# Kernel optimization log

Hardware: AMD Instinct MI355X
Metric: run time of the kernel (lower is better)

## Reference

```python
import jax, jax.numpy as jnp
import numpy as np

GROUPS = 32
EPS = 1e-5

def group_norm(x, w, b):
    # x: [B, C, T]
    B, C, T = x.shape
    g = x.reshape(B, GROUPS, C // GROUPS, T)
    mu = g.mean(axis=(2, 3), keepdims=True)
    var = g.var(axis=(2, 3), keepdims=True)
    g = (g - mu) * jax.lax.rsqrt(var + EPS)
    return g.reshape(B, C, T) * w[None, :, None] + b[None, :, None]

def conv1x1(x, w, b):
    # x: [B, C, T], w: [O, C], b: [O]
    return jnp.einsum('oc,bct->bot', w, x) + b[None, :, None]

def setup_inputs() -> dict:
    key = jax.random.key(0)
    ks = jax.random.split(key, 10)
    B, C, H, W = 128, 512, 16, 16
    d = {}
    d['criminal_cond'] = jax.random.normal(ks[0], (B, C, H, W), jnp.float32)
    d['morph_cond'] = jax.random.normal(ks[1], (B, C, H, W), jnp.float32)
    d['norm_w'] = jax.random.uniform(ks[2], (C,), jnp.float32, 0.5, 1.5)
    d['norm_b'] = 0.02 * jax.random.normal(ks[3], (C,), jnp.float32)
    d['qkv_w'] = jax.random.normal(ks[4], (3 * C, C), jnp.float32) / np.sqrt(C)
    d['qkv_b'] = 0.02 * jax.random.normal(ks[5], (3 * C,), jnp.float32)
    d['ekv_w'] = jax.random.normal(ks[6], (2 * C, C), jnp.float32) / np.sqrt(C)
    d['ekv_b'] = 0.02 * jax.random.normal(ks[7], (2 * C,), jnp.float32)
    d['proj_w'] = jax.random.normal(ks[8], (C, C), jnp.float32) / np.sqrt(C)
    d['proj_b'] = 0.02 * jax.random.normal(ks[9], (C,), jnp.float32)
    return d

def reference(criminal_cond, morph_cond, norm_w, norm_b, qkv_w, qkv_b, ekv_w, ekv_b, proj_w, proj_b):
    B, C, H, W = criminal_cond.shape
    x = criminal_cond.reshape(B, C, H * W)          # [B, C, T]
    cond = morph_cond.reshape(B, C, H * W)          # [B, C, S], S == T here
    h = group_norm(x, norm_w, norm_b)
    qkv = conv1x1(h, qkv_w, qkv_b)                  # [B, 3C, T]
    q, k, v = jnp.split(qkv, 3, axis=1)
    ekv = conv1x1(cond, ekv_w, ekv_b)               # [B, 2C, S]
    ek, ev = jnp.split(ekv, 2, axis=1)
    k = jnp.concatenate([ek, k], axis=-1)           # [B, C, S+T]
    v = jnp.concatenate([ev, v], axis=-1)
    scale = 1.0 / np.sqrt(np.sqrt(C))               # single head, head_dim = C
    logits = jnp.einsum('bct,bcs->bts', q * scale, k * scale)
    w = jax.nn.softmax(logits, axis=-1)             # [B, T, S+T]
    a = jnp.einsum('bts,bcs->bct', w, v)            # [B, C, T]
    hout = conv1x1(a, proj_w, proj_b)
    attn_out = (x + hout).reshape(B, C, H, W)
    return 2.0 * morph_cond - attn_out
```

## Files before the change

### kernel.cpp

```cpp
#include <hip/hip_runtime.h>
#include <hip/hip_bf16.h>
#include <math.h>

#define NB 128
#define NC 512
#define NT 256
#define NL 512
#define NG 32
#define SCALE2 0.04419417382415922f

typedef __attribute__((ext_vector_type(8))) short bf16x8;
typedef __attribute__((ext_vector_type(4))) float f32x4;
typedef __attribute__((ext_vector_type(4))) unsigned short u16x4;
typedef __attribute__((ext_vector_type(8))) unsigned short u16x8;
typedef __hip_bfloat16 bf16;

struct Params {
  const float *x, *morph, *qkvb, *ekvb, *projb;
  const bf16 *wq, *we, *wp;
  bf16 *hT, *mT, *qT, *kfT, *vf;
  float *out;
  int b0;
};

__device__ inline unsigned short f2bf_bits(float f) {
  bf16 h = __float2bfloat16(f);
  return *reinterpret_cast<unsigned short*>(&h);
}

__device__ inline void gld16(const void* g, void* lds) {
  __builtin_amdgcn_global_load_lds(
      (const __attribute__((address_space(1))) unsigned int*)g,
      (__attribute__((address_space(3))) unsigned int*)lds, 16, 0, 0);
}

__global__ __launch_bounds__(256) void gn_stats_k(const float* __restrict__ x,
                                                  float* __restrict__ stats) {
  const int bg = blockIdx.x;
  const float4* p4 = (const float4*)(x + (size_t)bg * 4096);
  float s = 0.f, s2 = 0.f;
  #pragma unroll
  for (int i = 0; i < 4; ++i) {
    float4 v = p4[threadIdx.x + i * 256];
    s  += v.x + v.y + v.z + v.w;
    s2 += v.x * v.x + v.y * v.y + v.z * v.z + v.w * v.w;
  }
  #pragma unroll
  for (int off = 32; off; off >>= 1) {
    s  += __shfl_down(s, off);
    s2 += __shfl_down(s2, off);
  }
  __shared__ float red[8];
  const int wave = threadIdx.x >> 6, lane = threadIdx.x & 63;
  if (lane == 0) { red[wave * 2] = s; red[wave * 2 + 1] = s2; }
  __syncthreads();
  if (threadIdx.x == 0) {
    float S = 0.f, S2 = 0.f;
    for (int w = 0; w < 4; ++w) { S += red[w * 2]; S2 += red[w * 2 + 1]; }
    float mu = S * (1.0f / 4096.0f);
    float var = S2 * (1.0f / 4096.0f) - mu * mu;
    stats[bg * 2]     = mu;
    stats[bg * 2 + 1] = rsqrtf(var + 1e-5f);
  }
}

__global__ __launch_bounds__(256) void cvt_k(const float* __restrict__ s,
                                             bf16* __restrict__ d, int n) {
  int i = blockIdx.x * 256 + threadIdx.x;
  if (i < n) d[i] = __float2bfloat16(s[i]);
}

__global__ __launch_bounds__(256) void transpose2_k(const float* __restrict__ x,
                                                    const float* __restrict__ morph,
                                                    bf16* __restrict__ hT,
                                                    bf16* __restrict__ mT,
                                                    const float* __restrict__ stats,
                                                    const float* __restrict__ gnw,
                                                    const float* __restrict__ gnb,
                                                    int b0, int nbc) {
  __shared__ float sm[64][65];
  const int z = blockIdx.z;
  const int norm = (z < nbc) ? 1 : 0;
  const int lb = norm ? z : z - nbc;
  const int gb = b0 + lb;
  const float* src = norm ? x : morph;
  bf16* dst = norm ? hT : mT;
  const int t0 = blockIdx.x * 64, c0 = blockIdx.y * 64;
  const int tx = threadIdx.x & 15, ty = threadIdx.x >> 4;
  #pragma unroll
  for (int ci = 0; ci < 4; ++ci) {
    const int c = ty + ci * 16;
    const int cg = c0 + c;
    float4 v = *(const float4*)&src[((size_t)gb * NC + cg) * NT + t0 + tx * 4];
    if (norm) {
      float mu = stats[(gb * NG + (cg >> 4)) * 2];
      float rs = stats[(gb * NG + (cg >> 4)) * 2 + 1];
      float wv = gnw[cg], bv = gnb[cg];
      v.x = (v.x - mu) * rs * wv + bv;
      v.y = (v.y - mu) * rs * wv + bv;
      v.z = (v.z - mu) * rs * wv + bv;
      v.w = (v.w - mu) * rs * wv + bv;
    }
    sm[c][tx * 4 + 0] = v.x; sm[c][tx * 4 + 1] = v.y;
    sm[c][tx * 4 + 2] = v.z; sm[c][tx * 4 + 3] = v.w;
  }
  __syncthreads();
  const int t = threadIdx.x >> 2, cq = threadIdx.x & 3;
  u16x8 pk0, pk1;
  #pragma unroll
  for (int k = 0; k < 8; ++k) pk0[k] = f2bf_bits(sm[cq * 16 + k][t]);
  #pragma unroll
  for (int k = 0; k < 8; ++k) pk1[k] = f2bf_bits(sm[cq * 16 + 8 + k][t]);
  bf16* d = dst + ((size_t)lb * NT + t0 + t) * NC + c0 + cq * 16;
  *(u16x8*)d = pk0;
  *(u16x8*)(d + 8) = pk1;
}

__global__ __launch_bounds__(256) void gemm_in_k(Params P) {
  __shared__ unsigned short As[128][32];
  __shared__ unsigned short Bs[128][32];
  const int lb = blockIdx.x;
  const int m0 = blockIdx.y * 128;
  const int z = blockIdx.z;
  const bool qkv = (z < 12);
  const int n0 = (qkv ? z : z - 12) * 128;
  const int tid = threadIdx.x;
  const int lane = tid & 63, w = tid >> 6;
  const int wr = w >> 1, wc = w & 1;
  const int ln = lane & 15, kq = lane >> 4;

  const bf16* Ab = (qkv ? P.hT : P.mT) + (size_t)lb * NT * NC;
  const bf16* Bb = qkv ? P.wq : P.we;

  const char* Abase = (const char*)(Ab + (size_t)m0 * 512);
  const char* Bbase = (const char*)(Bb + (size_t)n0 * 512);

  const int r_lo = w * 32 + (lane >> 2);
  const int cid16 = (lane & 3) * 16;

  f32x4 acc[4][4] = {};

  for (int k0 = 0; k0 < 512; k0 += 32) {
    const size_t kb = (size_t)k0 * 2 + cid16;
    #pragma unroll
    for (int h = 0; h < 2; ++h) {
      const int rw = r_lo + h * 16;
      gld16(Abase + (size_t)rw * 1024 + kb, (char*)As + w * 2048 + h * 1024);
      gld16(Bbase + (size_t)rw * 1024 + kb, (char*)Bs + w * 2048 + h * 1024);
    }
    __syncthreads();
    bf16x8 af[4], bfr[4];
    #pragma unroll
    for (int i = 0; i < 4; ++i)
      af[i] = *(const bf16x8*)&As[wr * 64 + i * 16 + ln][kq * 8];
    #pragma unroll
    for (int j = 0; j < 4; ++j)
      bfr[j] = *(const bf16x8*)&Bs[wc * 64 + j * 16 + ln][kq * 8];
    #pragma unroll
    for (int i = 0; i < 4; ++i)
      #pragma unroll
      for (int j = 0; j < 4; ++j)
        acc[i][j] = __builtin_amdgcn_mfma_f32_16x16x32_bf16(af[i], bfr[j], acc[i][j], 0, 0, 0);
    __syncthreads();
  }

  #pragma unroll
  for (int i = 0; i < 4; ++i) {
    const int ig = m0 + wr * 64 + i * 16 + kq * 4;
    #pragma unroll
    for (int j = 0; j < 4; ++j) {
      const int jg = n0 + wc * 64 + j * 16 + ln;
      f32x4 a = acc[i][j];
      if (qkv) {
        float bias = P.qkvb[jg];
        if (jg < 512) {
          bf16* d = P.qT + ((size_t)lb * NT + ig) * NC + jg;
          #pragma unroll
          for (int r = 0; r < 4; ++r) d[(size_t)r * NC] = __float2bfloat16(a[r] + bias);
        } else if (jg < 1024) {
          bf16* d = P.kfT + ((size_t)lb * NL + 256 + ig) * NC + (jg - 512);
          #pragma unroll
          for (int r = 0; r < 4; ++r) d[(size_t)r * NC] = __float2bfloat16(a[r] + bias);
        } else {
          u16x4 pk;
          #pragma unroll
          for (int r = 0; r < 4; ++r) pk[r] = f2bf_bits(a[r] + bias);
          *(u16x4*)(P.vf + ((size_t)lb * NC + (jg - 1024)) * NL + 256 + ig) = pk;
        }
      } else {
        float bias = P.ekvb[jg];
        if (jg < 512) {
          bf16* d = P.kfT + ((size_t)lb * NL + ig) * NC + jg;
          #pragma unroll
          for (int r = 0; r < 4; ++r) d[(size_t)r * NC] = __float2bfloat16(a[r] + bias);
        } else {
          u16x4 pk;
          #pragma unroll
          for (int r = 0; r < 4; ++r) pk[r] = f2bf_bits(a[r] + bias);
          *(u16x4*)(P.vf + ((size_t)lb * NC + (jg - 512)) * NL + ig) = pk;
        }
      }
    }
  }
}

__global__ __launch_bounds__(256) void att_sm_k(Params P) {
  __shared__ unsigned short Abuf[32][32];
  __shared__ unsigned short Bbuf[512][32];
  __shared__ float redm[4][32];
  __shared__ float reds[4][32];

  const int lb = blockIdx.x;
  const int t0 = blockIdx.y * 32;
  const int tid = threadIdx.x;
  const int lane = tid & 63, w = tid >> 6;
  const int ln = lane & 15, kq = lane >> 4;
  const int srow = lane >> 2;
  const int scol = (lane & 3) * 16;

  const char* qg = (const char*)(P.qT  + ((size_t)lb * NT + t0) * NC);
  const char* kg = (const char*)(P.kfT + (size_t)lb * NL * NC);

  f32x4 sa[2][8] = {};
  bf16x8 af[2], bfr[8];

  for (int k0 = 0; k0 < 512; k0 += 32) {
    const size_t koff = (size_t)k0 * 2 + scol;
    if (w < 2)
      gld16(qg + (size_t)(w * 16 + srow) * 1024 + koff, (char*)Abuf + w * 1024);
    #pragma unroll
    for (int h = 0; h < 8; ++h)
      gld16(kg + (size_t)(w * 128 + h * 16 + srow) * 1024 + koff,
            (char*)Bbuf + w * 8192 + h * 1024);
    __syncthreads();
    af[0] = *(const bf16x8*)&Abuf[ln][kq * 8];
    af[1] = *(const bf16x8*)&Abuf[16 + ln][kq * 8];
    #pragma unroll
    for (int j = 0; j < 8; ++j)
      bfr[j] = *(const bf16x8*)&Bbuf[w * 128 + j * 16 + ln][kq * 8];
    #pragma unroll
    for (int i = 0; i < 2; ++i)
      #pragma unroll
      for (int j = 0; j < 8; ++j)
        sa[i][j] = __builtin_amdgcn_mfma_f32_16x16x32_bf16(af[i], bfr[j], sa[i][j], 0, 0, 0);
    __syncthreads();
  }

  float mx[2][4], sum[2][4], inv[2][4];
  #pragma unroll
  for (int i = 0; i < 2; ++i)
    #pragma unroll
    for (int r = 0; r < 4; ++r) {
      float m = -1e30f;
      #pragma unroll
      for (int j = 0; j < 8; ++j) m = fmaxf(m, sa[i][j][r]);
      mx[i][r] = m;
    }
  #pragma unroll
  for (int off = 1; off < 16; off <<= 1)
    #pragma unroll
    for (int i = 0; i < 2; ++i)
      #pragma unroll
      for (int r = 0; r < 4; ++r) mx[i][r] = fmaxf(mx[i][r], __shfl_xor(mx[i][r], off));
  if (ln == 0)
    #pragma unroll
    for (int i = 0; i < 2; ++i)
      #pragma unroll
      for (int r = 0; r < 4; ++r) redm[w][i * 16 + kq * 4 + r] = mx[i][r];
  __syncthreads();
  #pragma unroll
  for (int i = 0; i < 2; ++i)
    #pragma unroll
    for (int r = 0; r < 4; ++r) {
      const int row = i * 16 + kq * 4 + r;
      mx[i][r] = fmaxf(fmaxf(redm[0][row], redm[1][row]),
                       fmaxf(redm[2][row], redm[3][row]));
      sum[i][r] = 0.f;
    }
  #pragma unroll
  for (int i = 0; i < 2; ++i)
    #pragma unroll
    for (int j = 0; j < 8; ++j)
      #pragma unroll
      for (int r = 0; r < 4; ++r) {
        float e = __expf(SCALE2 * (sa[i][j][r] - mx[i][r]));
        sa[i][j][r] = e;
        sum[i][r] += e;
      }
  #pragma unroll
  for (int off = 1; off < 16; off <<= 1)
    #pragma unroll
    for (int i = 0; i < 2; ++i)
      #pragma unroll
      for (int r = 0; r < 4; ++r) sum[i][r] += __shfl_xor(sum[i][r], off);
  if (ln == 0)
    #pragma unroll
    for (int i = 0; i < 2; ++i)
      #pragma unroll
      for (int r = 0; r < 4; ++r) reds[w][i * 16 + kq * 4 + r] = sum[i][r];
  __syncthreads();
  #pragma unroll
  for (int i = 0; i < 2; ++i)
    #pragma unroll
    for (int r = 0; r < 4; ++r) {
      const int row = i * 16 + kq * 4 + r;
      inv[i][r] = 1.0f / (reds[0][row] + reds[1][row] + reds[2][row] + reds[3][row]);
    }

  bf16* pdst = P.qT + ((size_t)lb * NT + t0) * NL;
  #pragma unroll
  for (int i = 0; i < 2; ++i)
    #pragma unroll
    for (int j = 0; j < 8; ++j)
      #pragma unroll
      for (int r = 0; r < 4; ++r)
        pdst[(size_t)(i * 16 + kq * 4 + r) * NL + w * 128 + j * 16 + ln] =
            __float2bfloat16(sa[i][j][r] * inv[i][r]);
}

template <int MODE>
__global__ __launch_bounds__(256) void gemm_att(Params P) {
  __shared__ unsigned short As[128][32];
  __shared__ unsigned short Bs[128][32];
  const int lb = blockIdx.x;
  const int m0 = blockIdx.y * 128;
  const int n0 = blockIdx.z * 128;
  const int tid = threadIdx.x;
  const int lane = tid & 63, w = tid >> 6;
  const int wr = w >> 1, wc = w & 1;
  const int ln = lane & 15, kq = lane >> 4;

  const bf16 *Ab, *Bb;
  if (MODE == 1) { Ab = P.qT  + (size_t)lb * 131072; Bb = P.vf + (size_t)lb * NC * NL; }
  else           { Ab = P.kfT + (size_t)lb * 262144; Bb = P.wp; }

  const char* Abase = (const char*)(Ab + (size_t)m0 * 512);
  const char* Bbase = (const char*)(Bb + (size_t)n0 * 512);

  const int r_lo = w * 32 + (lane >> 2);
  const int cid16 = (lane & 3) * 16;

  f32x4 acc[4][4] = {};

  for (int k0 = 0; k0 < 512; k0 += 32) {
    const size_t kb = (size_t)k0 * 2 + cid16;
    #pragma unroll
    for (int h = 0; h < 2; ++h) {
      const int rw = r_lo + h * 16;
      gld16(Abase + (size_t)rw * 1024 + kb, (char*)As + w * 2048 + h * 1024);
      gld16(Bbase + (size_t)rw * 1024 + kb, (char*)Bs + w * 2048 + h * 1024);
    }
    __syncthreads();
    bf16x8 af[4], bfr[4];
    #pragma unroll
    for (int i = 0; i < 4; ++i)
      af[i] = *(const bf16x8*)&As[wr * 64 + i * 16 + ln][kq * 8];
    #pragma unroll
    for (int j = 0; j < 4; ++j)
      bfr[j] = *(const bf16x8*)&Bs[wc * 64 + j * 16 + ln][kq * 8];
    #pragma unroll
    for (int i = 0; i < 4; ++i)
      #pragma unroll
      for (int j = 0; j < 4; ++j)
        acc[i][j] = __builtin_amdgcn_mfma_f32_16x16x32_bf16(af[i], bfr[j], acc[i][j], 0, 0, 0);
    __syncthreads();
  }

  bf16* Og = P.kfT + (size_t)lb * 262144;
  const int gb = P.b0 + lb;

  #pragma unroll
  for (int i = 0; i < 4; ++i) {
    const int ig = m0 + wr * 64 + i * 16 + kq * 4;
    #pragma unroll
    for (int j = 0; j < 4; ++j) {
      const int jg = n0 + wc * 64 + j * 16 + ln;
      f32x4 a = acc[i][j];
      if (MODE == 1) {
        bf16* d = Og + (size_t)ig * NC + jg;
        #pragma unroll
        for (int r = 0; r < 4; ++r) d[(size_t)r * NC] = __float2bfloat16(a[r]);
      } else {
        const float bias = P.projb[jg];
        const size_t idx = ((size_t)gb * NC + jg) * NT + ig;
        float4 mo = *(const float4*)&P.morph[idx];
        float4 xx = *(const float4*)&P.x[idx];
        f32x4 o;
        o[0] = 2.0f * mo.x - xx.x - (a[0] + bias);
        o[1] = 2.0f * mo.y - xx.y - (a[1] + bias);
        o[2] = 2.0f * mo.z - xx.z - (a[2] + bias);
        o[3] = 2.0f * mo.w - xx.w - (a[3] + bias);
        *(f32x4*)&P.out[idx] = o;
      }
    }
  }
}

extern "C" void kernel_launch(void* const* d_in, const int* in_sizes, int n_in,
                              void* d_out, int out_size, void* d_ws, size_t ws_size,
                              hipStream_t stream) {
  const float* x     = (const float*)d_in[0];
  const float* morph = (const float*)d_in[1];
  const float* gnw   = (const float*)d_in[2];
  const float* gnb   = (const float*)d_in[3];
  const float* qkvw  = (const float*)d_in[4];
  const float* qkvb  = (const float*)d_in[5];
  const float* ekvw  = (const float*)d_in[6];
  const float* ekvb  = (const float*)d_in[7];
  const float* projw = (const float*)d_in[8];
  const float* projb = (const float*)d_in[9];

  bf16* wq = (bf16*)d_ws;
  bf16* we = wq + 786432;
  bf16* wp = we + 524288;
  float* stats = (float*)(wp + 262144);
  bf16* pb = (bf16*)(stats + 8192);

  const size_t per_b = 917504;
  const size_t fixed = (size_t)(786432 + 524288 + 262144) * 2 + 8192 * 4;
  int nbc = NB;
  while (nbc > 1 && fixed + (size_t)nbc * per_b * 2 > ws_size) nbc >>= 1;

  Params P;
  P.x = x; P.morph = morph; P.qkvb = qkvb; P.ekvb = ekvb; P.projb = projb;
  P.wq = wq; P.we = we; P.wp = wp;
  P.hT  = pb;  pb += (size_t)nbc * 131072;
  P.mT  = pb;  pb += (size_t)nbc * 131072;
  P.qT  = pb;  pb += (size_t)nbc * 131072;
  P.kfT = pb;  pb += (size_t)nbc * 262144;
  P.vf  = pb;
  P.out = (float*)d_out;

  gn_stats_k<<<dim3(NB * NG), dim3(256), 0, stream>>>(x, stats);
  cvt_k<<<dim3(3072), dim3(256), 0, stream>>>(qkvw, wq, 786432);
  cvt_k<<<dim3(2048), dim3(256), 0, stream>>>(ekvw, we, 524288);
  cvt_k<<<dim3(1024), dim3(256), 0, stream>>>(projw, wp, 262144);

  for (int b0 = 0; b0 < NB; b0 += nbc) {
    P.b0 = b0;
    transpose2_k<<<dim3(4, 8, 2 * nbc), dim3(256), 0, stream>>>(
        x, morph, P.hT, P.mT, stats, gnw, gnb, b0, nbc);
    gemm_in_k  <<<dim3(nbc, 2, 20), dim3(256), 0, stream>>>(P);
    att_sm_k   <<<dim3(nbc, 8),     dim3(256), 0, stream>>>(P);
    gemm_att<1><<<dim3(nbc, 2, 4),  dim3(256), 0, stream>>>(P);
    gemm_att<2><<<dim3(nbc, 2, 4),  dim3(256), 0, stream>>>(P);
  }
}
```

Measured before the change: 537.0 us.

## Double-buffer LDS tiles in GEMM kernels to overlap global loads with MFMA

Result: slower. 565.7 us (+5.3%).

```diff
diff --git a/kernel.cpp b/kernel.cpp
--- a/kernel.cpp
+++ b/kernel.cpp
@@ -117,8 +117,8 @@
 }
 
 __global__ __launch_bounds__(256) void gemm_in_k(Params P) {
-  __shared__ unsigned short As[128][32];
-  __shared__ unsigned short Bs[128][32];
+  __shared__ unsigned short As[2][128][32];
+  __shared__ unsigned short Bs[2][128][32];
   const int lb = blockIdx.x;
   const int m0 = blockIdx.y * 128;
   const int z = blockIdx.z;
@@ -140,22 +140,33 @@
 
   f32x4 acc[4][4] = {};
 
-  for (int k0 = 0; k0 < 512; k0 += 32) {
-    const size_t kb = (size_t)k0 * 2 + cid16;
-    #pragma unroll
-    for (int h = 0; h < 2; ++h) {
-      const int rw = r_lo + h * 16;
-      gld16(Abase + (size_t)rw * 1024 + kb, (char*)As + w * 2048 + h * 1024);
-      gld16(Bbase + (size_t)rw * 1024 + kb, (char*)Bs + w * 2048 + h * 1024);
-    }
-    __syncthreads();
+  #pragma unroll
+  for (int h = 0; h < 2; ++h) {
+    const int rw = r_lo + h * 16;
+    gld16(Abase + (size_t)rw * 1024 + cid16, (char*)As[0] + w * 2048 + h * 1024);
+    gld16(Bbase + (size_t)rw * 1024 + cid16, (char*)Bs[0] + w * 2048 + h * 1024);
+  }
+  __syncthreads();
+
+  #pragma unroll
+  for (int t = 0; t < 16; ++t) {
+    const int cur = t & 1, nxt = cur ^ 1;
+    if (t < 15) {
+      const size_t kb = (size_t)(t + 1) * 64 + cid16;
+      #pragma unroll
+      for (int h = 0; h < 2; ++h) {
+        const int rw = r_lo + h * 16;
+        gld16(Abase + (size_t)rw * 1024 + kb, (char*)As[nxt] + w * 2048 + h * 1024);
+        gld16(Bbase + (size_t)rw * 1024 + kb, (char*)Bs[nxt] + w * 2048 + h * 1024);
+      }
+    }
     bf16x8 af[4], bfr[4];
     #pragma unroll
     for (int i = 0; i < 4; ++i)
-      af[i] = *(const bf16x8*)&As[wr * 64 + i * 16 + ln][kq * 8];
+      af[i] = *(const bf16x8*)&As[cur][wr * 64 + i * 16 + ln][kq * 8];
     #pragma unroll
     for (int j = 0; j < 4; ++j)
-      bfr[j] = *(const bf16x8*)&Bs[wc * 64 + j * 16 + ln][kq * 8];
+      bfr[j] = *(const bf16x8*)&Bs[cur][wc * 64 + j * 16 + ln][kq * 8];
     #pragma unroll
     for (int i = 0; i < 4; ++i)
       #pragma unroll
@@ -320,8 +331,8 @@
 
 template <int MODE>
 __global__ __launch_bounds__(256) void gemm_att(Params P) {
-  __shared__ unsigned short As[128][32];
-  __shared__ unsigned short Bs[128][32];
+  __shared__ unsigned short As[2][128][32];
+  __shared__ unsigned short Bs[2][128][32];
   const int lb = blockIdx.x;
   const int m0 = blockIdx.y * 128;
   const int n0 = blockIdx.z * 128;
@@ -342,22 +353,33 @@
 
   f32x4 acc[4][4] = {};
 
-  for (int k0 = 0; k0 < 512; k0 += 32) {
-    const size_t kb = (size_t)k0 * 2 + cid16;
-    #pragma unroll
-    for (int h = 0; h < 2; ++h) {
-      const int rw = r_lo + h * 16;
-      gld16(Abase + (size_t)rw * 1024 + kb, (char*)As + w * 2048 + h * 1024);
-      gld16(Bbase + (size_t)rw * 1024 + kb, (char*)Bs + w * 2048 + h * 1024);
-    }
-    __syncthreads();
+  #pragma unroll
+  for (int h = 0; h < 2; ++h) {
+    const int rw = r_lo + h * 16;
+    gld16(Abase + (size_t)rw * 1024 + cid16, (char*)As[0] + w * 2048 + h * 1024);
+    gld16(Bbase + (size_t)rw * 1024 + cid16, (char*)Bs[0] + w * 2048 + h * 1024);
+  }
+  __syncthreads();
+
+  #pragma unroll
+  for (int t = 0; t < 16; ++t) {
+    const int cur = t & 1, nxt = cur ^ 1;
+    if (t < 15) {
+      const size_t kb = (size_t)(t + 1) * 64 + cid16;
+      #pragma unroll
+      for (int h = 0; h < 2; ++h) {
+        const int rw = r_lo + h * 16;
+        gld16(Abase + (size_t)rw * 1024 + kb, (char*)As[nxt] + w * 2048 + h * 1024);
+        gld16(Bbase + (size_t)rw * 1024 + kb, (char*)Bs[nxt] + w * 2048 + h * 1024);
+      }
+    }
     bf16x8 af[4], bfr[4];
     #pragma unroll
     for (int i = 0; i < 4; ++i)
-      af[i] = *(const bf16x8*)&As[wr * 64 + i * 16 + ln][kq * 8];
+      af[i] = *(const bf16x8*)&As[cur][wr * 64 + i * 16 + ln][kq * 8];
     #pragma unroll
     for (int j = 0; j < 4; ++j)
-      bfr[j] = *(const bf16x8*)&Bs[wc * 64 + j * 16 + ln][kq * 8];
+      bfr[j] = *(const bf16x8*)&Bs[cur][wc * 64 + j * 16 + ln][kq * 8];
     #pragma unroll
     for (int i = 0; i < 4; ++i)
       #pragma unroll
```

## Double GEMM K-tile to 64 with XOR-swizzled LDS and fuse weight casts

Applied to the files above, without the earlier changes.

Result: slower. 553.5 us (+3.1%).

```diff
diff --git a/kernel.cpp b/kernel.cpp
--- a/kernel.cpp
+++ b/kernel.cpp
@@ -64,10 +64,18 @@
   }
 }
 
-__global__ __launch_bounds__(256) void cvt_k(const float* __restrict__ s,
-                                             bf16* __restrict__ d, int n) {
-  int i = blockIdx.x * 256 + threadIdx.x;
-  if (i < n) d[i] = __float2bfloat16(s[i]);
+__global__ __launch_bounds__(256) void cvt3_k(const float* __restrict__ a,
+                                              const float* __restrict__ b,
+                                              const float* __restrict__ c,
+                                              bf16* __restrict__ da,
+                                              bf16* __restrict__ db,
+                                              bf16* __restrict__ dc) {
+  const int i = blockIdx.x * 256 + threadIdx.x;
+  if (i < 786432) { da[i] = __float2bfloat16(a[i]); return; }
+  const int j = i - 786432;
+  if (j < 524288) { db[j] = __float2bfloat16(b[j]); return; }
+  const int k = j - 524288;
+  if (k < 262144) dc[k] = __float2bfloat16(c[k]);
 }
 
 __global__ __launch_bounds__(256) void transpose2_k(const float* __restrict__ x,
@@ -117,8 +125,8 @@
 }
 
 __global__ __launch_bounds__(256) void gemm_in_k(Params P) {
-  __shared__ unsigned short As[128][32];
-  __shared__ unsigned short Bs[128][32];
+  __shared__ unsigned short As[128][64];
+  __shared__ unsigned short Bs[128][64];
   const int lb = blockIdx.x;
   const int m0 = blockIdx.y * 128;
   const int z = blockIdx.z;
@@ -131,36 +139,40 @@
 
   const bf16* Ab = (qkv ? P.hT : P.mT) + (size_t)lb * NT * NC;
   const bf16* Bb = qkv ? P.wq : P.we;
-
   const char* Abase = (const char*)(Ab + (size_t)m0 * 512);
   const char* Bbase = (const char*)(Bb + (size_t)n0 * 512);
 
-  const int r_lo = w * 32 + (lane >> 2);
-  const int cid16 = (lane & 3) * 16;
+  const int r8 = lane >> 3;
+  const int ssl = (lane & 7) ^ r8;
+  const int xr = ln & 7;
 
   f32x4 acc[4][4] = {};
 
-  for (int k0 = 0; k0 < 512; k0 += 32) {
-    const size_t kb = (size_t)k0 * 2 + cid16;
-    #pragma unroll
-    for (int h = 0; h < 2; ++h) {
-      const int rw = r_lo + h * 16;
-      gld16(Abase + (size_t)rw * 1024 + kb, (char*)As + w * 2048 + h * 1024);
-      gld16(Bbase + (size_t)rw * 1024 + kb, (char*)Bs + w * 2048 + h * 1024);
-    }
-    __syncthreads();
-    bf16x8 af[4], bfr[4];
-    #pragma unroll
-    for (int i = 0; i < 4; ++i)
-      af[i] = *(const bf16x8*)&As[wr * 64 + i * 16 + ln][kq * 8];
-    #pragma unroll
-    for (int j = 0; j < 4; ++j)
-      bfr[j] = *(const bf16x8*)&Bs[wc * 64 + j * 16 + ln][kq * 8];
-    #pragma unroll
-    for (int i = 0; i < 4; ++i)
+  for (int k0 = 0; k0 < 512; k0 += 64) {
+    #pragma unroll
+    for (int h = 0; h < 4; ++h) {
+      const int rw = w * 32 + h * 8 + r8;
+      const size_t goff = (size_t)rw * 1024 + (size_t)k0 * 2 + ssl * 16;
+      gld16(Abase + goff, (char*)As + (w * 32 + h * 8) * 128);
+      gld16(Bbase + goff, (char*)Bs + (w * 32 + h * 8) * 128);
+    }
+    __syncthreads();
+    #pragma unroll
+    for (int hf = 0; hf < 2; ++hf) {
+      const int sl = ((hf * 4 + kq) ^ xr) * 8;
+      bf16x8 af[4], bfr[4];
+      #pragma unroll
+      for (int i = 0; i < 4; ++i)
+        af[i] = *(const bf16x8*)&As[wr * 64 + i * 16 + ln][sl];
       #pragma unroll
       for (int j = 0; j < 4; ++j)
-        acc[i][j] = __builtin_amdgcn_mfma_f32_16x16x32_bf16(af[i], bfr[j], acc[i][j], 0, 0, 0);
+        bfr[j] = *(const bf16x8*)&Bs[wc * 64 + j * 16 + ln][sl];
+      #pragma unroll
+      for (int i = 0; i < 4; ++i)
+        #pragma unroll
+        for (int j = 0; j < 4; ++j)
+          acc[i][j] = __builtin_amdgcn_mfma_f32_16x16x32_bf16(af[i], bfr[j], acc[i][j], 0, 0, 0);
+    }
     __syncthreads();
   }
 
@@ -320,8 +332,8 @@
 
 template <int MODE>
 __global__ __launch_bounds__(256) void gemm_att(Params P) {
-  __shared__ unsigned short As[128][32];
-  __shared__ unsigned short Bs[128][32];
+  __shared__ unsigned short As[128][64];
+  __shared__ unsigned short Bs[128][64];
   const int lb = blockIdx.x;
   const int m0 = blockIdx.y * 128;
   const int n0 = blockIdx.z * 128;
@@ -337,32 +349,37 @@
   const char* Abase = (const char*)(Ab + (size_t)m0 * 512);
   const char* Bbase = (const char*)(Bb + (size_t)n0 * 512);
 
-  const int r_lo = w * 32 + (lane >> 2);
-  const int cid16 = (lane & 3) * 16;
+  const int r8 = lane >> 3;
+  const int ssl = (lane & 7) ^ r8;
+  const int xr = ln & 7;
 
   f32x4 acc[4][4] = {};
 
-  for (int k0 = 0; k0 < 512; k0 += 32) {
-    const size_t kb = (size_t)k0 * 2 + cid16;
-    #pragma unroll
-    for (int h = 0; h < 2; ++h) {
-      const int rw = r_lo + h * 16;
-      gld16(Abase + (size_t)rw * 1024 + kb, (char*)As + w * 2048 + h * 1024);
-      gld16(Bbase + (size_t)rw * 1024 + kb, (char*)Bs + w * 2048 + h * 1024);
-    }
-    __syncthreads();
-    bf16x8 af[4], bfr[4];
-    #pragma unroll
-    for (int i = 0; i < 4; ++i)
-      af[i] = *(const bf16x8*)&As[wr * 64 + i * 16 + ln][kq * 8];
-    #pragma unroll
-    for (int j = 0; j < 4; ++j)
-      bfr[j] = *(const bf16x8*)&Bs[wc * 64 + j * 16 + ln][kq * 8];
-    #pragma unroll
-    for (int i = 0; i < 4; ++i)
+  for (int k0 = 0; k0 < 512; k0 += 64) {
+    #pragma unroll
+    for (int h = 0; h < 4; ++h) {
+      const int rw = w * 32 + h * 8 + r8;
+      const size_t goff = (size_t)rw * 1024 + (size_t)k0 * 2 + ssl * 16;
+      gld16(Abase + goff, (char*)As + (w * 32 + h * 8) * 128);
+      gld16(Bbase + goff, (char*)Bs + (w * 32 + h * 8) * 128);
+    }
+    __syncthreads();
+    #pragma unroll
+    for (int hf = 0; hf < 2; ++hf) {
+      const int sl = ((hf * 4 + kq) ^ xr) * 8;
+      bf16x8 af[4], bfr[4];
+      #pragma unroll
+      for (int i = 0; i < 4; ++i)
+        af[i] = *(const bf16x8*)&As[wr * 64 + i * 16 + ln][sl];
       #pragma unroll
       for (int j = 0; j < 4; ++j)
-        acc[i][j] = __builtin_amdgcn_mfma_f32_16x16x32_bf16(af[i], bfr[j], acc[i][j], 0, 0, 0);
+        bfr[j] = *(const bf16x8*)&Bs[wc * 64 + j * 16 + ln][sl];
+      #pragma unroll
+      for (int i = 0; i < 4; ++i)
+        #pragma unroll
+        for (int j = 0; j < 4; ++j)
+          acc[i][j] = __builtin_amdgcn_mfma_f32_16x16x32_bf16(af[i], bfr[j], acc[i][j], 0, 0, 0);
+    }
     __syncthreads();
   }
 
@@ -432,9 +449,7 @@
   P.out = (float*)d_out;
 
   gn_stats_k<<<dim3(NB * NG), dim3(256), 0, stream>>>(x, stats);
-  cvt_k<<<dim3(3072), dim3(256), 0, stream>>>(qkvw, wq, 786432);
-  cvt_k<<<dim3(2048), dim3(256), 0, stream>>>(ekvw, we, 524288);
-  cvt_k<<<dim3(1024), dim3(256), 0, stream>>>(projw, wp, 262144);
+  cvt3_k<<<dim3(6144), dim3(256), 0, stream>>>(qkvw, ekvw, projw, wq, we, wp);
 
   for (int b0 = 0; b0 < NB; b0 += nbc) {
     P.b0 = b0;
```

## Widen GEMM tiles to 128x256 and merge prep kernels into one launch

Applied to the files above, without the earlier changes.

New measurement: 667.0 us. 24.2% more time.

```diff
diff --git a/kernel.cpp b/kernel.cpp
--- a/kernel.cpp
+++ b/kernel.cpp
@@ -34,40 +34,49 @@
       (__attribute__((address_space(3))) unsigned int*)lds, 16, 0, 0);
 }
 
-__global__ __launch_bounds__(256) void gn_stats_k(const float* __restrict__ x,
-                                                  float* __restrict__ stats) {
-  const int bg = blockIdx.x;
-  const float4* p4 = (const float4*)(x + (size_t)bg * 4096);
-  float s = 0.f, s2 = 0.f;
-  #pragma unroll
-  for (int i = 0; i < 4; ++i) {
-    float4 v = p4[threadIdx.x + i * 256];
-    s  += v.x + v.y + v.z + v.w;
-    s2 += v.x * v.x + v.y * v.y + v.z * v.z + v.w * v.w;
-  }
-  #pragma unroll
-  for (int off = 32; off; off >>= 1) {
-    s  += __shfl_down(s, off);
-    s2 += __shfl_down(s2, off);
-  }
-  __shared__ float red[8];
-  const int wave = threadIdx.x >> 6, lane = threadIdx.x & 63;
-  if (lane == 0) { red[wave * 2] = s; red[wave * 2 + 1] = s2; }
-  __syncthreads();
-  if (threadIdx.x == 0) {
-    float S = 0.f, S2 = 0.f;
-    for (int w = 0; w < 4; ++w) { S += red[w * 2]; S2 += red[w * 2 + 1]; }
-    float mu = S * (1.0f / 4096.0f);
-    float var = S2 * (1.0f / 4096.0f) - mu * mu;
-    stats[bg * 2]     = mu;
-    stats[bg * 2 + 1] = rsqrtf(var + 1e-5f);
-  }
-}
-
-__global__ __launch_bounds__(256) void cvt_k(const float* __restrict__ s,
-                                             bf16* __restrict__ d, int n) {
-  int i = blockIdx.x * 256 + threadIdx.x;
-  if (i < n) d[i] = __float2bfloat16(s[i]);
+__global__ __launch_bounds__(256) void prep_k(const float* __restrict__ x,
+                                              float* __restrict__ stats,
+                                              const float* __restrict__ wa,
+                                              const float* __restrict__ wb,
+                                              const float* __restrict__ wc,
+                                              bf16* __restrict__ da,
+                                              bf16* __restrict__ db,
+                                              bf16* __restrict__ dc) {
+  if (blockIdx.x < 4096) {
+    const int bg = blockIdx.x;
+    const float4* p4 = (const float4*)(x + (size_t)bg * 4096);
+    float s = 0.f, s2 = 0.f;
+    #pragma unroll
+    for (int i = 0; i < 4; ++i) {
+      float4 v = p4[threadIdx.x + i * 256];
+      s  += v.x + v.y + v.z + v.w;
+      s2 += v.x * v.x + v.y * v.y + v.z * v.z + v.w * v.w;
+    }
+    #pragma unroll
+    for (int off = 32; off; off >>= 1) {
+      s  += __shfl_down(s, off);
+      s2 += __shfl_down(s2, off);
+    }
+    __shared__ float red[8];
+    const int wave = threadIdx.x >> 6, lane = threadIdx.x & 63;
+    if (lane == 0) { red[wave * 2] = s; red[wave * 2 + 1] = s2; }
+    __syncthreads();
+    if (threadIdx.x == 0) {
+      float S = 0.f, S2 = 0.f;
+      for (int w = 0; w < 4; ++w) { S += red[w * 2]; S2 += red[w * 2 + 1]; }
+      float mu = S * (1.0f / 4096.0f);
+      float var = S2 * (1.0f / 4096.0f) - mu * mu;
+      stats[bg * 2]     = mu;
+      stats[bg * 2 + 1] = rsqrtf(var + 1e-5f);
+    }
+  } else {
+    const int i = (blockIdx.x - 4096) * 256 + threadIdx.x;
+    if (i < 786432) { da[i] = __float2bfloat16(wa[i]); return; }
+    const int j = i - 786432;
+    if (j < 524288) { db[j] = __float2bfloat16(wb[j]); return; }
+    const int k = j - 524288;
+    if (k < 262144) dc[k] = __float2bfloat16(wc[k]);
+  }
 }
 
 __global__ __launch_bounds__(256) void transpose2_k(const float* __restrict__ x,
@@ -118,12 +127,12 @@
 
 __global__ __launch_bounds__(256) void gemm_in_k(Params P) {
   __shared__ unsigned short As[128][32];
-  __shared__ unsigned short Bs[128][32];
+  __shared__ unsigned short Bs[2][128][32];
   const int lb = blockIdx.x;
   const int m0 = blockIdx.y * 128;
   const int z = blockIdx.z;
-  const bool qkv = (z < 12);
-  const int n0 = (qkv ? z : z - 12) * 128;
+  const bool qkv = (z < 6);
+  const int n0 = (qkv ? z : z - 6) * 256;
   const int tid = threadIdx.x;
   const int lane = tid & 63, w = tid >> 6;
   const int wr = w >> 1, wc = w & 1;
@@ -131,14 +140,13 @@
 
   const bf16* Ab = (qkv ? P.hT : P.mT) + (size_t)lb * NT * NC;
   const bf16* Bb = qkv ? P.wq : P.we;
-
   const char* Abase = (const char*)(Ab + (size_t)m0 * 512);
   const char* Bbase = (const char*)(Bb + (size_t)n0 * 512);
 
   const int r_lo = w * 32 + (lane >> 2);
   const int cid16 = (lane & 3) * 16;
 
-  f32x4 acc[4][4] = {};
+  f32x4 acc[2][4][4] = {};
 
   for (int k0 = 0; k0 < 512; k0 += 32) {
     const size_t kb = (size_t)k0 * 2 + cid16;
@@ -146,7 +154,10 @@
     for (int h = 0; h < 2; ++h) {
       const int rw = r_lo + h * 16;
       gld16(Abase + (size_t)rw * 1024 + kb, (char*)As + w * 2048 + h * 1024);
-      gld16(Bbase + (size_t)rw * 1024 + kb, (char*)Bs + w * 2048 + h * 1024);
+      #pragma unroll
+      for (int nb = 0; nb < 2; ++nb)
+        gld16(Bbase + (size_t)(nb * 128 + rw) * 1024 + kb,
+              (char*)Bs[nb] + w * 2048 + h * 1024);
     }
     __syncthreads();
     bf16x8 af[4], bfr[4];
@@ -154,50 +165,56 @@
     for (int i = 0; i < 4; ++i)
       af[i] = *(const bf16x8*)&As[wr * 64 + i * 16 + ln][kq * 8];
     #pragma unroll
-    for (int j = 0; j < 4; ++j)
-      bfr[j] = *(const bf16x8*)&Bs[wc * 64 + j * 16 + ln][kq * 8];
-    #pragma unroll
-    for (int i = 0; i < 4; ++i)
+    for (int nb = 0; nb < 2; ++nb) {
       #pragma unroll
       for (int j = 0; j < 4; ++j)
-        acc[i][j] = __builtin_amdgcn_mfma_f32_16x16x32_bf16(af[i], bfr[j], acc[i][j], 0, 0, 0);
-    __syncthreads();
-  }
-
-  #pragma unroll
-  for (int i = 0; i < 4; ++i) {
-    const int ig = m0 + wr * 64 + i * 16 + kq * 4;
-    #pragma unroll
-    for (int j = 0; j < 4; ++j) {
-      const int jg = n0 + wc * 64 + j * 16 + ln;
-      f32x4 a = acc[i][j];
-      if (qkv) {
-        float bias = P.qkvb[jg];
-        if (jg < 512) {
-          bf16* d = P.qT + ((size_t)lb * NT + ig) * NC + jg;
-          #pragma unroll
-          for (int r = 0; r < 4; ++r) d[(size_t)r * NC] = __float2bfloat16(a[r] + bias);
-        } else if (jg < 1024) {
-          bf16* d = P.kfT + ((size_t)lb * NL + 256 + ig) * NC + (jg - 512);
-          #pragma unroll
-          for (int r = 0; r < 4; ++r) d[(size_t)r * NC] = __float2bfloat16(a[r] + bias);
+        bfr[j] = *(const bf16x8*)&Bs[nb][wc * 64 + j * 16 + ln][kq * 8];
+      #pragma unroll
+      for (int i = 0; i < 4; ++i)
+        #pragma unroll
+        for (int j = 0; j < 4; ++j)
+          acc[nb][i][j] = __builtin_amdgcn_mfma_f32_16x16x32_bf16(af[i], bfr[j], acc[nb][i][j], 0, 0, 0);
+    }
+    __syncthreads();
+  }
+
+  #pragma unroll
+  for (int nb = 0; nb < 2; ++nb) {
+    #pragma unroll
+    for (int i = 0; i < 4; ++i) {
+      const int ig = m0 + wr * 64 + i * 16 + kq * 4;
+      #pragma unroll
+      for (int j = 0; j < 4; ++j) {
+        const int jg = n0 + nb * 128 + wc * 64 + j * 16 + ln;
+        f32x4 a = acc[nb][i][j];
+        if (qkv) {
+          float bias = P.qkvb[jg];
+          if (jg < 512) {
+            bf16* d = P.qT + ((size_t)lb * NT + ig) * NC + jg;
+            #pragma unroll
+            for (int r = 0; r < 4; ++r) d[(size_t)r * NC] = __float2bfloat16(a[r] + bias);
+          } else if (jg < 1024) {
+            bf16* d = P.kfT + ((size_t)lb * NL + 256 + ig) * NC + (jg - 512);
+            #pragma unroll
+            for (int r = 0; r < 4; ++r) d[(size_t)r * NC] = __float2bfloat16(a[r] + bias);
+          } else {
+            u16x4 pk;
+            #pragma unroll
+            for (int r = 0; r < 4; ++r) pk[r] = f2bf_bits(a[r] + bias);
+            *(u16x4*)(P.vf + ((size_t)lb * NC + (jg - 1024)) * NL + 256 + ig) = pk;
+          }
         } else {
-          u16x4 pk;
-          #pragma unroll
-          for (int r = 0; r < 4; ++r) pk[r] = f2bf_bits(a[r] + bias);
-          *(u16x4*)(P.vf + ((size_t)lb * NC + (jg - 1024)) * NL + 256 + ig) = pk;
-        }
-      } else {
-        float bias = P.ekvb[jg];
-        if (jg < 512) {
-          bf16* d = P.kfT + ((size_t)lb * NL + ig) * NC + jg;
-          #pragma unroll
-          for (int r = 0; r < 4; ++r) d[(size_t)r * NC] = __float2bfloat16(a[r] + bias);
-        } else {
-          u16x4 pk;
-          #pragma unroll
-          for (int r = 0; r < 4; ++r) pk[r] = f2bf_bits(a[r] + bias);
-          *(u16x4*)(P.vf + ((size_t)lb * NC + (jg - 512)) * NL + ig) = pk;
+          float bias = P.ekvb[jg];
+          if (jg < 512) {
+            bf16* d = P.kfT + ((size_t)lb * NL + ig) * NC + jg;
+            #pragma unroll
+            for (int r = 0; r < 4; ++r) d[(size_t)r * NC] = __float2bfloat16(a[r] + bias);
+          } else {
+            u16x4 pk;
+            #pragma unroll
+            for (int r = 0; r < 4; ++r) pk[r] = f2bf_bits(a[r] + bias);
+            *(u16x4*)(P.vf + ((size_t)lb * NC + (jg - 512)) * NL + ig) = pk;
+          }
         }
       }
     }
@@ -321,10 +338,10 @@
 template <int MODE>
 __global__ __launch_bounds__(256) void gemm_att(Params P) {
   __shared__ unsigned short As[128][32];
-  __shared__ unsigned short Bs[128][32];
+  __shared__ unsigned short Bs[2][128][32];
   const int lb = blockIdx.x;
   const int m0 = blockIdx.y * 128;
-  const int n0 = blockIdx.z * 128;
+  const int n0 = blockIdx.z * 256;
   const int tid = threadIdx.x;
   const int lane = tid & 63, w = tid >> 6;
   const int wr = w >> 1, wc = w & 1;
@@ -340,7 +357,7 @@
   const int r_lo = w * 32 + (lane >> 2);
   const int cid16 = (lane & 3) * 16;
 
-  f32x4 acc[4][4] = {};
+  f32x4 acc[2][4][4] = {};
 
   for (int k0 = 0; k0 < 512; k0 += 32) {
     const size_t kb = (size_t)k0 * 2 + cid16;
@@ -348,7 +365,10 @@
     for (int h = 0; h < 2; ++h) {
       const int rw = r_lo + h * 16;
       gld16(Abase + (size_t)rw * 1024 + kb, (char*)As + w * 2048 + h * 1024);
-      gld16(Bbase + (size_t)rw * 1024 + kb, (char*)Bs + w * 2048 + h * 1024);
+      #pragma unroll
+      for (int nb = 0; nb < 2; ++nb)
+        gld16(Bbase + (size_t)(nb * 128 + rw) * 1024 + kb,
+              (char*)Bs[nb] + w * 2048 + h * 1024);
     }
     __syncthreads();
     bf16x8 af[4], bfr[4];
@@ -356,13 +376,16 @@
     for (int i = 0; i < 4; ++i)
       af[i] = *(const bf16x8*)&As[wr * 64 + i * 16 + ln][kq * 8];
     #pragma unroll
-    for (int j = 0; j < 4; ++j)
-      bfr[j] = *(const bf16x8*)&Bs[wc * 64 + j * 16 + ln][kq * 8];
-    #pragma unroll
-    for (int i = 0; i < 4; ++i)
+    for (int nb = 0; nb < 2; ++nb) {
       #pragma unroll
       for (int j = 0; j < 4; ++j)
-        acc[i][j] = __builtin_amdgcn_mfma_f32_16x16x32_bf16(af[i], bfr[j], acc[i][j], 0, 0, 0);
+        bfr[j] = *(const bf16x8*)&Bs[nb][wc * 64 + j * 16 + ln][kq * 8];
+      #pragma unroll
+      for (int i = 0; i < 4; ++i)
+        #pragma unroll
+        for (int j = 0; j < 4; ++j)
+          acc[nb][i][j] = __builtin_amdgcn_mfma_f32_16x16x32_bf16(af[i], bfr[j], acc[nb][i][j], 0, 0, 0);
+    }
     __syncthreads();
   }
 
@@ -370,27 +393,30 @@
   const int gb = P.b0 + lb;
 
   #pragma unroll
-  for (int i = 0; i < 4; ++i) {
-    const int ig = m0 + wr * 64 + i * 16 + kq * 4;
-    #pragma unroll
-    for (int j = 0; j < 4; ++j) {
-      const int jg = n0 + wc * 64 + j * 16 + ln;
-      f32x4 a = acc[i][j];
-      if (MODE == 1) {
-        bf16* d = Og + (size_t)ig * NC + jg;
-        #pragma unroll
-        for (int r = 0; r < 4; ++r) d[(size_t)r * NC] = __float2bfloat16(a[r]);
-      } else {
-        const float bias = P.projb[jg];
-        const size_t idx = ((size_t)gb * NC + jg) * NT + ig;
-        float4 mo = *(const float4*)&P.morph[idx];
-        float4 xx = *(const float4*)&P.x[idx];
-        f32x4 o;
-        o[0] = 2.0f * mo.x - xx.x - (a[0] + bias);
-        o[1] = 2.0f * mo.y - xx.y - (a[1] + bias);
-        o[2] = 2.0f * mo.z - xx.z - (a[2] + bias);
-        o[3] = 2.0f * mo.w - xx.w - (a[3] + bias);
-        *(f32x4*)&P.out[idx] = o;
+  for (int nb = 0; nb < 2; ++nb) {
+    #pragma unroll
+    for (int i = 0; i < 4; ++i) {
+      const int ig = m0 + wr * 64 + i * 16 + kq * 4;
+      #pragma unroll
+      for (int j = 0; j < 4; ++j) {
+        const int jg = n0 + nb * 128 + wc * 64 + j * 16 + ln;
+        f32x4 a = acc[nb][i][j];
+        if (MODE == 1) {
+          bf16* d = Og + (size_t)ig * NC + jg;
+          #pragma unroll
+          for (int r = 0; r < 4; ++r) d[(size_t)r * NC] = __float2bfloat16(a[r]);
+        } else {
+          const float bias = P.projb[jg];
+          const size_t idx = ((size_t)gb * NC + jg) * NT + ig;
+          float4 mo = *(const float4*)&P.morph[idx];
+          float4 xx = *(const float4*)&P.x[idx];
+          f32x4 o;
+          o[0] = 2.0f * mo.x - xx.x - (a[0] + bias);
+          o[1] = 2.0f * mo.y - xx.y - (a[1] + bias);
+          o[2] = 2.0f * mo.z - xx.z - (a[2] + bias);
+          o[3] = 2.0f * mo.w - xx.w - (a[3] + bias);
+          *(f32x4*)&P.out[idx] = o;
+        }
       }
     }
   }
@@ -431,18 +457,15 @@
   P.vf  = pb;
   P.out = (float*)d_out;
 
-  gn_stats_k<<<dim3(NB * NG), dim3(256), 0, stream>>>(x, stats);
-  cvt_k<<<dim3(3072), dim3(256), 0, stream>>>(qkvw, wq, 786432);
-  cvt_k<<<dim3(2048), dim3(256), 0, stream>>>(ekvw, we, 524288);
-  cvt_k<<<dim3(1024), dim3(256), 0, stream>>>(projw, wp, 262144);
+  prep_k<<<dim3(10240), dim3(256), 0, stream>>>(x, stats, qkvw, ekvw, projw, wq, we, wp);
 
   for (int b0 = 0; b0 < NB; b0 += nbc) {
     P.b0 = b0;
     transpose2_k<<<dim3(4, 8, 2 * nbc), dim3(256), 0, stream>>>(
         x, morph, P.hT, P.mT, stats, gnw, gnb, b0, nbc);
-    gemm_in_k  <<<dim3(nbc, 2, 20), dim3(256), 0, stream>>>(P);
+    gemm_in_k  <<<dim3(nbc, 2, 10), dim3(256), 0, stream>>>(P);
     att_sm_k   <<<dim3(nbc, 8),     dim3(256), 0, stream>>>(P);
-    gemm_att<1><<<dim3(nbc, 2, 4),  dim3(256), 0, stream>>>(P);
-    gemm_att<2><<<dim3(nbc, 2, 4),  dim3(256), 0, stream>>>(P);
-  }
-}
+    gemm_att<1><<<dim3(nbc, 2, 2),  dim3(256), 0, stream>>>(P);
+    gemm_att<2><<<dim3(nbc, 2, 2),  dim3(256), 0, stream>>>(P);
+  }
+}
```
